# Kernel tuning notes

Measured on AMD Instinct MI355X. Metric: run time of the kernel, lower is better.

Reference implementation:

```python
import jax, jax.numpy as jnp
import numpy as np

SQRT_2_OVER_PI = 0.7978845608028654

def gelu_new(x):
    # HF 'gelu_new': 0.5*x*(1+tanh(sqrt(2/pi)*(x+0.044715*x^3)))
    return 0.5 * x * (1.0 + jnp.tanh(SQRT_2_OVER_PI * (x + 0.044715 * x * x * x)))

def phm_linear(x, phm_rule, W_left, W_right, bias, n):
    # x: [..., n*p]; phm_rule: [n, n, n]; W_left: [n, p, r]; W_right: [n, r, q]
    # H = sum_i kron(phm_rule[i], W_i), W_i = W_left[i] @ W_right[i]; y = x @ H + b
    p = x.shape[-1] // n
    W = jnp.einsum('ipk,ikq->ipq', W_left, W_right)          # [n, p, q]
    xr = x.reshape(x.shape[:-1] + (n, p))                    # [..., n, p]
    # kron(A,B)[a*p+r, c*q+s] = A[a,c]*B[r,s]
    y = jnp.einsum('...ap,iac,ipq->...cq', xr, phm_rule, W)  # [..., n, q]
    y = y.reshape(x.shape[:-1] + (n * W.shape[-1],))
    return y + bias

def setup_inputs() -> dict:
    key = jax.random.key(0)
    ks = jax.random.split(key, 7)
    B, S, D, d, n = 8, 4096, 768, 192, 4
    x = jax.random.normal(ks[0], (B, S, D), dtype=jnp.float32)
    phm_rule_d = jax.random.normal(ks[1], (n, n, n), dtype=jnp.float32) * 0.01
    W_left_d = jax.random.normal(ks[2], (n, D // n, 1), dtype=jnp.float32) * 0.05
    W_right_d = jax.random.normal(ks[3], (n, 1, d // n), dtype=jnp.float32) * 0.05
    bias_d = jnp.zeros((d,), dtype=jnp.float32)
    phm_rule_u = jax.random.normal(ks[4], (n, n, n), dtype=jnp.float32) * 0.01
    W_left_u = jax.random.normal(ks[5], (n, d // n, 1), dtype=jnp.float32) * 0.05
    W_right_u = jax.random.normal(ks[6], (n, 1, D // n), dtype=jnp.float32) * 0.05
    bias_u = jnp.zeros((D,), dtype=jnp.float32)
    return {"x": x, "phm_rule_d": phm_rule_d, "W_left_d": W_left_d, "W_right_d": W_right_d,
            "bias_d": bias_d, "phm_rule_u": phm_rule_u, "W_left_u": W_left_u,
            "W_right_u": W_right_u, "bias_u": bias_u}

def reference(x, phm_rule_d, W_left_d, W_right_d, bias_d, phm_rule_u, W_left_u, W_right_u, bias_u):
    n = phm_rule_d.shape[0]
    z = phm_linear(x, phm_rule_d, W_left_d, W_right_d, bias_d, n)
    z = gelu_new(z)
    return phm_linear(z, phm_rule_u, W_left_u, W_right_u, bias_u, n)
```

## Files before the change

### kernel.cpp

```cpp
#include <hip/hip_runtime.h>
#include <math.h>


#define SQ2PI 0.79788456080286535588f
#define T_TILE 8

template<int CTRL>
__device__ __forceinline__ float ror_add(float v) {
    int s = __builtin_amdgcn_update_dpp(0, __float_as_int(v), CTRL, 0xF, 0xF, true);
    return v + __int_as_float(s);
}
__device__ __forceinline__ float reduce16(float v) {
    v = ror_add<0x121>(v);
    v = ror_add<0x122>(v);
    v = ror_add<0x124>(v);
    v = ror_add<0x128>(v);
    return v;
}

__global__ __launch_bounds__(256, 4)
void phm_fused(const float* __restrict__ x,
               const float* __restrict__ rule_d,
               const float* __restrict__ Wl_d,
               const float* __restrict__ Wr_d,
               const float* __restrict__ bias_d,
               const float* __restrict__ rule_u,
               const float* __restrict__ Wl_u,
               const float* __restrict__ Wr_u,
               const float* __restrict__ bias_u,
               float* __restrict__ out,
               int n_tokens)
{
    __shared__ __attribute__((aligned(16))) float sTile[T_TILE * 768];
    __shared__ __attribute__((aligned(16))) float sLd[768];
    __shared__ __attribute__((aligned(16))) float sRu[768];
    __shared__ __attribute__((aligned(16))) float sBu[768];

    const int tid = threadIdx.x;
    for (int i = tid; i < 768; i += 256) sLd[i] = Wl_d[i];
    for (int i = tid; i < 768; i += 256) sRu[i] = Wr_u[i];
    for (int i = tid; i < 768; i += 256) sBu[i] = bias_u[i];

    const int lane = tid & 63;
    const int wave = tid >> 6;
    const int a    = lane >> 4;
    const int r    = lane & 15;

    float rD[4][4], rU[4][4];
    #pragma unroll
    for (int k = 0; k < 4; ++k)
        #pragma unroll
        for (int i = 0; i < 4; ++i) {
            rD[k][i] = rule_d[i*16 + (a^k)*4 + a];
            rU[k][i] = rule_u[i*16 + (a^k)*4 + a];
        }
    float lu[4][3];
    #pragma unroll
    for (int i = 0; i < 4; ++i)
        #pragma unroll
        for (int w = 0; w < 3; ++w) lu[i][w] = Wl_u[i*48 + 3*r + w];
    float bd[3];
    float rdw[4][3];
    #pragma unroll
    for (int w = 0; w < 3; ++w) bd[w] = bias_d[a*48 + 3*r + w];
    #pragma unroll
    for (int i = 0; i < 4; ++i)
        #pragma unroll
        for (int w = 0; w < 3; ++w) rdw[i][w] = Wr_d[i*48 + 3*r + w];

    __syncthreads();

    const long long total4 = (long long)n_tokens * 192;
    const int n_tiles = (n_tokens + T_TILE - 1) / T_TILE;

    for (int tile = blockIdx.x; tile < n_tiles; tile += gridDim.x) {
        const long long g4 = (long long)tile * (T_TILE * 192);

        #pragma unroll
        for (int j = 0; j < (T_TILE * 192) / 256; ++j) {
            const int idx = tid + j * 256;
            const long long gi = g4 + idx;
            float4 v = make_float4(0.f, 0.f, 0.f, 0.f);
            if (gi < total4) v = *(const float4*)(x + gi * 4);
            *(float4*)&sTile[idx * 4] = v;
        }
        __syncthreads();

        float* xt0 = &sTile[(wave*2) * 768 + a*192 + 12*r];
        float* xt1 = xt0 + 768;
        float4 xv0[3], xv1[3];
        #pragma unroll
        for (int u = 0; u < 3; ++u) {
            xv0[u] = *(const float4*)(xt0 + 4*u);
            xv1[u] = *(const float4*)(xt1 + 4*u);
        }

        float sd0[4], sd1[4];
        #pragma unroll
        for (int i = 0; i < 4; ++i) {
            float a0 = 0.f, a1 = 0.f;
            #pragma unroll
            for (int u = 0; u < 3; ++u) {
                const float4 lv = *(const float4*)(&sLd[i*192 + 12*r + 4*u]);
                a0 = fmaf(xv0[u].x, lv.x, a0);  a1 = fmaf(xv1[u].x, lv.x, a1);
                a0 = fmaf(xv0[u].y, lv.y, a0);  a1 = fmaf(xv1[u].y, lv.y, a1);
                a0 = fmaf(xv0[u].z, lv.z, a0);  a1 = fmaf(xv1[u].z, lv.z, a1);
                a0 = fmaf(xv0[u].w, lv.w, a0);  a1 = fmaf(xv1[u].w, lv.w, a1);
            }
            sd0[i] = reduce16(a0);
            sd1[i] = reduce16(a1);
        }

        float tD0[4], tD1[4];
        #pragma unroll
        for (int i = 0; i < 4; ++i) {
            float x1 = __shfl_xor(sd0[i], 16);
            float x2 = __shfl_xor(sd0[i], 32);
            float x3 = __shfl_xor(x1,     32);
            tD0[i] = fmaf(sd0[i], rD[0][i], fmaf(x1, rD[1][i],
                     fmaf(x2,     rD[2][i],      x3 * rD[3][i])));
            x1 = __shfl_xor(sd1[i], 16);
            x2 = __shfl_xor(sd1[i], 32);
            x3 = __shfl_xor(x1,     32);
            tD1[i] = fmaf(sd1[i], rD[0][i], fmaf(x1, rD[1][i],
                     fmaf(x2,     rD[2][i],      x3 * rD[3][i])));
        }

        float g0[3], g1[3];
        #pragma unroll
        for (int w = 0; w < 3; ++w) {
            float z0 = bd[w], z1 = bd[w];
            #pragma unroll
            for (int i = 0; i < 4; ++i) {
                z0 = fmaf(tD0[i], rdw[i][w], z0);
                z1 = fmaf(tD1[i], rdw[i][w], z1);
            }
            const float i0 = SQ2PI * fmaf(0.044715f*z0, z0*z0, z0);
            const float i1 = SQ2PI * fmaf(0.044715f*z1, z1*z1, z1);
            const float e0 = __expf(2.0f*i0);
            const float e1 = __expf(2.0f*i1);
            g0[w] = 0.5f*z0*(1.0f + (1.0f - 2.0f/(e0 + 1.0f)));
            g1[w] = 0.5f*z1*(1.0f + (1.0f - 2.0f/(e1 + 1.0f)));
        }

        float tU0[4], tU1[4];
        #pragma unroll
        for (int i = 0; i < 4; ++i) {
            float a0 = 0.f, a1 = 0.f;
            #pragma unroll
            for (int w = 0; w < 3; ++w) {
                a0 = fmaf(g0[w], lu[i][w], a0);
                a1 = fmaf(g1[w], lu[i][w], a1);
            }
            const float h0 = reduce16(a0);
            const float h1 = reduce16(a1);
            float x1 = __shfl_xor(h0, 16);
            float x2 = __shfl_xor(h0, 32);
            float x3 = __shfl_xor(x1, 32);
            tU0[i] = fmaf(h0, rU[0][i], fmaf(x1, rU[1][i],
                     fmaf(x2, rU[2][i],      x3 * rU[3][i])));
            x1 = __shfl_xor(h1, 16);
            x2 = __shfl_xor(h1, 32);
            x3 = __shfl_xor(x1, 32);
            tU1[i] = fmaf(h1, rU[0][i], fmaf(x1, rU[1][i],
                     fmaf(x2, rU[2][i],      x3 * rU[3][i])));
        }

        #pragma unroll
        for (int u = 0; u < 3; ++u) {
            const float4 b = *(const float4*)(&sBu[a*192 + 12*r + 4*u]);
            float4 ov0 = b, ov1 = b;
            #pragma unroll
            for (int i = 0; i < 4; ++i) {
                const float4 ru = *(const float4*)(&sRu[i*192 + 12*r + 4*u]);
                ov0.x = fmaf(tU0[i], ru.x, ov0.x);  ov1.x = fmaf(tU1[i], ru.x, ov1.x);
                ov0.y = fmaf(tU0[i], ru.y, ov0.y);  ov1.y = fmaf(tU1[i], ru.y, ov1.y);
                ov0.z = fmaf(tU0[i], ru.z, ov0.z);  ov1.z = fmaf(tU1[i], ru.z, ov1.z);
                ov0.w = fmaf(tU0[i], ru.w, ov0.w);  ov1.w = fmaf(tU1[i], ru.w, ov1.w);
            }
            *(float4*)(xt0 + 4*u) = ov0;
            *(float4*)(xt1 + 4*u) = ov1;
        }
        __syncthreads();

        #pragma unroll
        for (int j = 0; j < (T_TILE * 192) / 256; ++j) {
            const int idx = tid + j * 256;
            const long long gi = g4 + idx;
            if (gi < total4)
                *(float4*)(out + gi * 4) = *(const float4*)&sTile[idx * 4];
        }
        __syncthreads();
    }
}

extern "C" void kernel_launch(void* const* d_in, const int* in_sizes, int n_in,
                              void* d_out, int out_size, void* d_ws, size_t ws_size,
                              hipStream_t stream) {
    const float* x      = (const float*)d_in[0];
    const float* rule_d = (const float*)d_in[1];
    const float* Wl_d   = (const float*)d_in[2];
    const float* Wr_d   = (const float*)d_in[3];
    const float* bias_d = (const float*)d_in[4];
    const float* rule_u = (const float*)d_in[5];
    const float* Wl_u   = (const float*)d_in[6];
    const float* Wr_u   = (const float*)d_in[7];
    const float* bias_u = (const float*)d_in[8];
    float* out          = (float*)d_out;

    const int n_tokens = in_sizes[0] / 768;

    phm_fused<<<dim3(1024), dim3(256), 0, stream>>>(
        x, rule_d, Wl_d, Wr_d, bias_d, rule_u, Wl_u, Wr_u, bias_u, out, n_tokens);
}
```

Before: 207.1 us.

## Give each wave its own token-pair staging buffer and drop block barriers

Each wave now loads, computes and stores its own pair of tokens through a private shared-memory slice. This removes the three block-wide __syncthreads per tile and lets waves progress independently. It also moves the rule and Wl_u tables from registers into shared memory and keeps bias_u in registers, and relaxes the launch bound to trade register pressure against occupancy. Odd token counts and tail handling are no longer guarded, and the per-wave loop has no barrier or fence between the load, compute and store phases on the same buffer, which relies on intra-wave ordering.

```diff
diff --git a/kernel.cpp b/kernel.cpp
--- a/kernel.cpp
+++ b/kernel.cpp
@@ -3,7 +3,6 @@
 
 
 #define SQ2PI 0.79788456080286535588f
-#define T_TILE 8
 
 template<int CTRL>
 __device__ __forceinline__ float ror_add(float v) {
@@ -18,7 +17,7 @@
     return v;
 }
 
-__global__ __launch_bounds__(256, 4)
+__global__ __launch_bounds__(256)
 void phm_fused(const float* __restrict__ x,
                const float* __restrict__ rule_d,
                const float* __restrict__ Wl_d,
@@ -31,99 +30,82 @@
                float* __restrict__ out,
                int n_tokens)
 {
-    __shared__ __attribute__((aligned(16))) float sTile[T_TILE * 768];
+    __shared__ __attribute__((aligned(16))) float sW[4][1536];
     __shared__ __attribute__((aligned(16))) float sLd[768];
     __shared__ __attribute__((aligned(16))) float sRu[768];
-    __shared__ __attribute__((aligned(16))) float sBu[768];
+    __shared__ __attribute__((aligned(16))) float sLu[192];
+    __shared__ float sRuleD[64];
+    __shared__ float sRuleU[64];
 
     const int tid = threadIdx.x;
     for (int i = tid; i < 768; i += 256) sLd[i] = Wl_d[i];
     for (int i = tid; i < 768; i += 256) sRu[i] = Wr_u[i];
-    for (int i = tid; i < 768; i += 256) sBu[i] = bias_u[i];
+    if (tid < 192)      sLu[tid]        = Wl_u[tid];
+    if (tid < 64)       sRuleD[tid]     = rule_d[tid];
+    else if (tid < 128) sRuleU[tid-64]  = rule_u[tid-64];
 
     const int lane = tid & 63;
     const int wave = tid >> 6;
     const int a    = lane >> 4;
     const int r    = lane & 15;
 
-    float rD[4][4], rU[4][4];
-    #pragma unroll
-    for (int k = 0; k < 4; ++k)
-        #pragma unroll
-        for (int i = 0; i < 4; ++i) {
-            rD[k][i] = rule_d[i*16 + (a^k)*4 + a];
-            rU[k][i] = rule_u[i*16 + (a^k)*4 + a];
-        }
-    float lu[4][3];
-    #pragma unroll
-    for (int i = 0; i < 4; ++i)
-        #pragma unroll
-        for (int w = 0; w < 3; ++w) lu[i][w] = Wl_u[i*48 + 3*r + w];
     float bd[3];
     float rdw[4][3];
+    float4 bu[3];
     #pragma unroll
     for (int w = 0; w < 3; ++w) bd[w] = bias_d[a*48 + 3*r + w];
     #pragma unroll
     for (int i = 0; i < 4; ++i)
         #pragma unroll
         for (int w = 0; w < 3; ++w) rdw[i][w] = Wr_d[i*48 + 3*r + w];
+    #pragma unroll
+    for (int u = 0; u < 3; ++u)
+        bu[u] = *(const float4*)(bias_u + a*192 + 12*r + 4*u);
 
     __syncthreads();
 
-    const long long total4 = (long long)n_tokens * 192;
-    const int n_tiles = (n_tokens + T_TILE - 1) / T_TILE;
+    float* W = sW[wave];
+    const int wid     = blockIdx.x * 4 + wave;
+    const int n_waves = gridDim.x * 4;
+    const int n_pairs = n_tokens >> 1;
 
-    for (int tile = blockIdx.x; tile < n_tiles; tile += gridDim.x) {
-        const long long g4 = (long long)tile * (T_TILE * 192);
+    for (int pr = wid; pr < n_pairs; pr += n_waves) {
+        const float* xp = x + (size_t)pr * 1536;
 
         #pragma unroll
-        for (int j = 0; j < (T_TILE * 192) / 256; ++j) {
-            const int idx = tid + j * 256;
-            const long long gi = g4 + idx;
-            float4 v = make_float4(0.f, 0.f, 0.f, 0.f);
-            if (gi < total4) v = *(const float4*)(x + gi * 4);
-            *(float4*)&sTile[idx * 4] = v;
+        for (int j = 0; j < 6; ++j) {
+            const float4 v = *(const float4*)(xp + (lane + 64*j) * 4);
+            *(float4*)&W[(lane + 64*j) * 4] = v;
         }
-        __syncthreads();
 
-        float* xt0 = &sTile[(wave*2) * 768 + a*192 + 12*r];
-        float* xt1 = xt0 + 768;
-        float4 xv0[3], xv1[3];
+        float s0[4] = {0,0,0,0}, s1[4] = {0,0,0,0};
         #pragma unroll
         for (int u = 0; u < 3; ++u) {
-            xv0[u] = *(const float4*)(xt0 + 4*u);
-            xv1[u] = *(const float4*)(xt1 + 4*u);
-        }
-
-        float sd0[4], sd1[4];
-        #pragma unroll
-        for (int i = 0; i < 4; ++i) {
-            float a0 = 0.f, a1 = 0.f;
+            const float4 xa = *(const float4*)&W[      a*192 + 12*r + 4*u];
+            const float4 xb = *(const float4*)&W[768 + a*192 + 12*r + 4*u];
             #pragma unroll
-            for (int u = 0; u < 3; ++u) {
-                const float4 lv = *(const float4*)(&sLd[i*192 + 12*r + 4*u]);
-                a0 = fmaf(xv0[u].x, lv.x, a0);  a1 = fmaf(xv1[u].x, lv.x, a1);
-                a0 = fmaf(xv0[u].y, lv.y, a0);  a1 = fmaf(xv1[u].y, lv.y, a1);
-                a0 = fmaf(xv0[u].z, lv.z, a0);  a1 = fmaf(xv1[u].z, lv.z, a1);
-                a0 = fmaf(xv0[u].w, lv.w, a0);  a1 = fmaf(xv1[u].w, lv.w, a1);
+            for (int i = 0; i < 4; ++i) {
+                const float4 lv = *(const float4*)&sLd[i*192 + 12*r + 4*u];
+                s0[i] = fmaf(xa.x, lv.x, s0[i]);  s1[i] = fmaf(xb.x, lv.x, s1[i]);
+                s0[i] = fmaf(xa.y, lv.y, s0[i]);  s1[i] = fmaf(xb.y, lv.y, s1[i]);
+                s0[i] = fmaf(xa.z, lv.z, s0[i]);  s1[i] = fmaf(xb.z, lv.z, s1[i]);
+                s0[i] = fmaf(xa.w, lv.w, s0[i]);  s1[i] = fmaf(xb.w, lv.w, s1[i]);
             }
-            sd0[i] = reduce16(a0);
-            sd1[i] = reduce16(a1);
         }
 
         float tD0[4], tD1[4];
         #pragma unroll
         for (int i = 0; i < 4; ++i) {
-            float x1 = __shfl_xor(sd0[i], 16);
-            float x2 = __shfl_xor(sd0[i], 32);
-            float x3 = __shfl_xor(x1,     32);
-            tD0[i] = fmaf(sd0[i], rD[0][i], fmaf(x1, rD[1][i],
-                     fmaf(x2,     rD[2][i],      x3 * rD[3][i])));
-            x1 = __shfl_xor(sd1[i], 16);
-            x2 = __shfl_xor(sd1[i], 32);
-            x3 = __shfl_xor(x1,     32);
-            tD1[i] = fmaf(sd1[i], rD[0][i], fmaf(x1, rD[1][i],
-                     fmaf(x2,     rD[2][i],      x3 * rD[3][i])));
+            const float rk0 = sRuleD[i*16 + (a^0)*4 + a];
+            const float rk1 = sRuleD[i*16 + (a^1)*4 + a];
+            const float rk2 = sRuleD[i*16 + (a^2)*4 + a];
+            const float rk3 = sRuleD[i*16 + (a^3)*4 + a];
+            const float h0 = reduce16(s0[i]);
+            const float h1 = reduce16(s1[i]);
+            float x1 = __shfl_xor(h0, 16), x2 = __shfl_xor(h0, 32), x3 = __shfl_xor(x1, 32);
+            tD0[i] = fmaf(h0, rk0, fmaf(x1, rk1, fmaf(x2, rk2, x3 * rk3)));
+            x1 = __shfl_xor(h1, 16); x2 = __shfl_xor(h1, 32); x3 = __shfl_xor(x1, 32);
+            tD1[i] = fmaf(h1, rk0, fmaf(x1, rk1, fmaf(x2, rk2, x3 * rk3)));
         }
 
         float g0[3], g1[3];
@@ -146,51 +128,44 @@
         float tU0[4], tU1[4];
         #pragma unroll
         for (int i = 0; i < 4; ++i) {
-            float a0 = 0.f, a1 = 0.f;
-            #pragma unroll
-            for (int w = 0; w < 3; ++w) {
-                a0 = fmaf(g0[w], lu[i][w], a0);
-                a1 = fmaf(g1[w], lu[i][w], a1);
-            }
+            const float l0 = sLu[i*48 + 3*r + 0];
+            const float l1 = sLu[i*48 + 3*r + 1];
+            const float l2 = sLu[i*48 + 3*r + 2];
+            const float rk0 = sRuleU[i*16 + (a^0)*4 + a];
+            const float rk1 = sRuleU[i*16 + (a^1)*4 + a];
+            const float rk2 = sRuleU[i*16 + (a^2)*4 + a];
+            const float rk3 = sRuleU[i*16 + (a^3)*4 + a];
+            float a0 = g0[0]*l0 + g0[1]*l1 + g0[2]*l2;
+            float a1 = g1[0]*l0 + g1[1]*l1 + g1[2]*l2;
             const float h0 = reduce16(a0);
             const float h1 = reduce16(a1);
-            float x1 = __shfl_xor(h0, 16);
-            float x2 = __shfl_xor(h0, 32);
-            float x3 = __shfl_xor(x1, 32);
-            tU0[i] = fmaf(h0, rU[0][i], fmaf(x1, rU[1][i],
-                     fmaf(x2, rU[2][i],      x3 * rU[3][i])));
-            x1 = __shfl_xor(h1, 16);
-            x2 = __shfl_xor(h1, 32);
-            x3 = __shfl_xor(x1, 32);
-            tU1[i] = fmaf(h1, rU[0][i], fmaf(x1, rU[1][i],
-                     fmaf(x2, rU[2][i],      x3 * rU[3][i])));
+            float x1 = __shfl_xor(h0, 16), x2 = __shfl_xor(h0, 32), x3 = __shfl_xor(x1, 32);
+            tU0[i] = fmaf(h0, rk0, fmaf(x1, rk1, fmaf(x2, rk2, x3 * rk3)));
+            x1 = __shfl_xor(h1, 16); x2 = __shfl_xor(h1, 32); x3 = __shfl_xor(x1, 32);
+            tU1[i] = fmaf(h1, rk0, fmaf(x1, rk1, fmaf(x2, rk2, x3 * rk3)));
         }
 
         #pragma unroll
         for (int u = 0; u < 3; ++u) {
-            const float4 b = *(const float4*)(&sBu[a*192 + 12*r + 4*u]);
-            float4 ov0 = b, ov1 = b;
+            float4 ov0 = bu[u], ov1 = bu[u];
             #pragma unroll
             for (int i = 0; i < 4; ++i) {
-                const float4 ru = *(const float4*)(&sRu[i*192 + 12*r + 4*u]);
+                const float4 ru = *(const float4*)&sRu[i*192 + 12*r + 4*u];
                 ov0.x = fmaf(tU0[i], ru.x, ov0.x);  ov1.x = fmaf(tU1[i], ru.x, ov1.x);
                 ov0.y = fmaf(tU0[i], ru.y, ov0.y);  ov1.y = fmaf(tU1[i], ru.y, ov1.y);
                 ov0.z = fmaf(tU0[i], ru.z, ov0.z);  ov1.z = fmaf(tU1[i], ru.z, ov1.z);
                 ov0.w = fmaf(tU0[i], ru.w, ov0.w);  ov1.w = fmaf(tU1[i], ru.w, ov1.w);
             }
-            *(float4*)(xt0 + 4*u) = ov0;
-            *(float4*)(xt1 + 4*u) = ov1;
+            *(float4*)&W[      a*192 + 12*r + 4*u] = ov0;
+            *(float4*)&W[768 + a*192 + 12*r + 4*u] = ov1;
         }
-        __syncthreads();
 
+        float* op = out + (size_t)pr * 1536;
         #pragma unroll
-        for (int j = 0; j < (T_TILE * 192) / 256; ++j) {
-            const int idx = tid + j * 256;
-            const long long gi = g4 + idx;
-            if (gi < total4)
-                *(float4*)(out + gi * 4) = *(const float4*)&sTile[idx * 4];
+        for (int j = 0; j < 6; ++j) {
+            const float4 v = *(const float4*)&W[(lane + 64*j) * 4];
+            *(float4*)(op + (lane + 64*j) * 4) = v;
         }
-        __syncthreads();
     }
 }
 
```

After: 192.2 us. 7.2% less time.
